# Optimization experiments

Measured on AMD Instinct MI355X. Metric: run time of the kernel, lower is better.

## Reference

```python
import jax, jax.numpy as jnp
import numpy as np

F_NODES = 16384   # number of function nodes
DEG = 8           # in-degree == out-degree per function node
E = F_NODES * DEG # edge-latent dimension (num edges)
B = 64            # batch
H = 16            # hidden_channels of each per-node MLP
LAYERS = 10       # GSNN layers (weights shared across layers)


def setup_inputs() -> dict:
    key = jax.random.key(0)
    k0, k1, k2, k3 = jax.random.split(key, 4)
    x0 = jax.random.normal(k0, (B, E), dtype=jnp.float32)
    # each edge has exactly one destination function node -> in_ixs is a permutation of edges
    in_ixs = jax.random.permutation(k1, E).reshape(F_NODES, DEG)
    # per-node 2-layer MLP weights: in_degree -> H -> out_degree
    W1 = jax.random.normal(k2, (F_NODES, H, DEG), dtype=jnp.float32) * (1.0 / np.sqrt(DEG))
    b1 = jnp.zeros((F_NODES, H), dtype=jnp.float32)
    W2 = jax.random.normal(k3, (F_NODES, DEG, H), dtype=jnp.float32) * (1.0 / np.sqrt(H))
    b2 = jnp.zeros((F_NODES, DEG), dtype=jnp.float32)
    return {"x0": x0, "W1": W1, "b1": b1, "W2": W2, "b2": b2, "in_ixs": in_ixs}


def reference(x0, W1, b1, W2, b2, in_ixs):
    # x0: [B, E] edge-latent input. Each layer: every function node gathers its
    # in-edges, applies its own small MLP, scatters to its out-edges; results are
    # summed into x_new and a residual x0 is added (GSNN.forward).
    x = x0
    for _ in range(LAYERS):
        g = x[:, in_ixs]                                   # [B, F, DEG] gather in-edge values
        h = jax.nn.elu(jnp.einsum('bfd,fhd->bfh', g, W1) + b1)  # [B, F, H]
        o = jnp.einsum('bfh,foh->bfo', h, W2) + b2         # [B, F, DEG]
        # out-edges of node f are the contiguous slots f*DEG:(f+1)*DEG (disjoint scatter)
        x = o.reshape(x0.shape) + x0                       # sum of node scatters + residual
    return x
```

## Files before the change

### kernel.cpp

```cpp
#include <hip/hip_runtime.h>
#include <math.h>

#define F_NODES 16384
#define DEG 8
#define E_TOT (F_NODES * DEG)
#define B 64
#define H 16
#define LAYERS 10
#define NPW 2

typedef unsigned short bf16_t;

__device__ __forceinline__ bf16_t f32_to_bf16(float f)
{
    unsigned u = __float_as_uint(f);
    u = (u + 0x7FFFu + ((u >> 16) & 1u)) >> 16;
    return (bf16_t)u;
}
__device__ __forceinline__ float bf16_to_f32(bf16_t h)
{
    return __uint_as_float((unsigned)h << 16);
}
__device__ __forceinline__ float bfu_lo(unsigned u) { return __uint_as_float(u << 16); }
__device__ __forceinline__ float bfu_hi(unsigned u) { return __uint_as_float(u & 0xFFFF0000u); }

__device__ __forceinline__ float fast_elu(float x)
{
    float e = __builtin_amdgcn_exp2f(x * 1.44269504088896340736f) - 1.0f;
    return x > 0.0f ? x : e;
}

__global__ __launch_bounds__(256) void transpose_in_kernel(
    const float* __restrict__ x0, bf16_t* __restrict__ xT16)
{
    __shared__ float tile[64 * 65];
    const int e0 = blockIdx.x * 64;
    const int c  = threadIdx.x & 63;
    const int r  = threadIdx.x >> 6;

    #pragma unroll
    for (int i = 0; i < 16; ++i) {
        const int b = r + i * 4;
        tile[c * 65 + b] = x0[(size_t)b * E_TOT + e0 + c];
    }
    __syncthreads();
    const int b = threadIdx.x & 63;
    #pragma unroll
    for (int i = 0; i < 16; ++i) {
        const int el = r + i * 4;
        xT16[(size_t)(e0 + el) * B + b] = f32_to_bf16(tile[el * 65 + b]);
    }
}

__global__ __launch_bounds__(256) void build_inv_kernel(
    const int* __restrict__ in_ixs, int* __restrict__ inv)
{
    const int k = blockIdx.x * 256 + threadIdx.x;
    inv[in_ixs[k]] = k;
}

__global__ __launch_bounds__(256) void pack_weights_kernel(
    const float* __restrict__ W1, const float* __restrict__ W2,
    unsigned* __restrict__ W1b, unsigned* __restrict__ W2b)
{
    const int i = blockIdx.x * 256 + threadIdx.x;
    float2 a = ((const float2*)W1)[i];
    W1b[i] = (unsigned)f32_to_bf16(a.x) | ((unsigned)f32_to_bf16(a.y) << 16);
    float2 c = ((const float2*)W2)[i];
    W2b[i] = (unsigned)f32_to_bf16(c.x) | ((unsigned)f32_to_bf16(c.y) << 16);
}

template <int MODE>
__global__ __launch_bounds__(256) void layer_kernel(
    const bf16_t*  __restrict__ zin,
    const bf16_t*  __restrict__ x0T16,
    const unsigned* __restrict__ W1b,
    const float*   __restrict__ b1,
    const unsigned* __restrict__ W2b,
    const float*   __restrict__ b2,
    const int*     __restrict__ in_ixs,
    const int*     __restrict__ inv,
    bf16_t* __restrict__ zout,
    float*  __restrict__ out)
{
    const int lane    = threadIdx.x & 63;
    const int wv      = threadIdx.x >> 6;
    const int wave_id = (int)blockIdx.x * 4 + wv;
    const int f0      = __builtin_amdgcn_readfirstlane(wave_id * NPW);

    float g[NPW][DEG], r[NPW][DEG];
    {
        if (MODE == 0) {
            const int* ixp = in_ixs + f0 * DEG;
            #pragma unroll
            for (int n = 0; n < NPW; ++n)
                #pragma unroll
                for (int d = 0; d < DEG; ++d)
                    g[n][d] = bf16_to_f32(
                        x0T16[(size_t)ixp[n * DEG + d] * B + lane]);
        } else {
            const bf16_t* zp = zin + (size_t)f0 * DEG * B + lane;
            #pragma unroll
            for (int n = 0; n < NPW; ++n)
                #pragma unroll
                for (int d = 0; d < DEG; ++d)
                    g[n][d] = bf16_to_f32(zp[(n * DEG + d) * B]);
        }
        const bf16_t* rp = x0T16 + (size_t)f0 * DEG * B + lane;
        #pragma unroll
        for (int n = 0; n < NPW; ++n)
            #pragma unroll
            for (int d = 0; d < DEG; ++d)
                r[n][d] = bf16_to_f32(rp[(n * DEG + d) * B]);
    }

    #pragma unroll
    for (int n = 0; n < NPW; ++n) {
        const int f = f0 + n;

        const unsigned* w1 = W1b + f * (H * DEG / 2);
        const float*   bb1 = b1 + f * H;
        float h[H];
        #pragma unroll
        for (int j = 0; j < H; ++j) {
            float acc = bb1[j];
            #pragma unroll
            for (int dp = 0; dp < DEG / 2; ++dp) {
                const unsigned u = w1[j * (DEG / 2) + dp];
                acc = fmaf(bfu_lo(u), g[n][2 * dp],     acc);
                acc = fmaf(bfu_hi(u), g[n][2 * dp + 1], acc);
            }
            h[j] = fast_elu(acc);
        }

        const unsigned* w2 = W2b + f * (DEG * H / 2);
        const float*   bb2 = b2 + f * DEG;
        float o[DEG];
        #pragma unroll
        for (int d = 0; d < DEG; ++d) {
            float acc = bb2[d];
            #pragma unroll
            for (int jp = 0; jp < H / 2; ++jp) {
                const unsigned u = w2[d * (H / 2) + jp];
                acc = fmaf(bfu_lo(u), h[2 * jp],     acc);
                acc = fmaf(bfu_hi(u), h[2 * jp + 1], acc);
            }
            o[d] = acc + r[n][d];
        }

        if (MODE == 2) {
            float4 v0 = make_float4(o[0], o[1], o[2], o[3]);
            float4 v1 = make_float4(o[4], o[5], o[6], o[7]);
            float4* dst = (float4*)(out + (size_t)lane * E_TOT + f * DEG);
            dst[0] = v0;
            dst[1] = v1;
        } else {
            const int* invp = inv + f * DEG;
            #pragma unroll
            for (int d = 0; d < DEG; ++d)
                zout[(size_t)invp[d] * B + lane] = f32_to_bf16(o[d]);
        }
    }
}

extern "C" void kernel_launch(void* const* d_in, const int* in_sizes, int n_in,
                              void* d_out, int out_size, void* d_ws, size_t ws_size,
                              hipStream_t stream)
{
    const float* x0     = (const float*)d_in[0];
    const float* W1     = (const float*)d_in[1];
    const float* b1     = (const float*)d_in[2];
    const float* W2     = (const float*)d_in[3];
    const float* b2     = (const float*)d_in[4];
    const int*   in_ixs = (const int*)d_in[5];
    float* out = (float*)d_out;

    const size_t NEL = (size_t)E_TOT * B;
    bf16_t*   x0T16 = (bf16_t*)d_ws;
    bf16_t*   zA    = x0T16 + NEL;
    bf16_t*   zB    = zA + NEL;
    int*      inv   = (int*)(zB + NEL);
    unsigned* W1b   = (unsigned*)(inv + E_TOT);
    unsigned* W2b   = W1b + F_NODES * H * DEG / 2;

    transpose_in_kernel<<<E_TOT / 64, 256, 0, stream>>>(x0, x0T16);
    build_inv_kernel<<<E_TOT / 256, 256, 0, stream>>>(in_ixs, inv);
    pack_weights_kernel<<<F_NODES * H * DEG / 2 / 256, 256, 0, stream>>>(
        W1, W2, W1b, W2b);

    const int grid = F_NODES / (4 * NPW);

    layer_kernel<0><<<grid, 256, 0, stream>>>(
        nullptr, x0T16, W1b, b1, W2b, b2, in_ixs, inv, zA, nullptr);

    const bf16_t* cur = zA;
    bf16_t* nxt = zB;
    for (int l = 1; l < LAYERS - 1; ++l) {
        layer_kernel<1><<<grid, 256, 0, stream>>>(
            cur, x0T16, W1b, b1, W2b, b2, in_ixs, inv, nxt, nullptr);
        cur = nxt;
        nxt = (nxt == zA) ? zB : zA;
    }

    layer_kernel<2><<<grid, 256, 0, stream>>>(
        cur, x0T16, W1b, b1, W2b, b2, in_ixs, inv, nullptr, out);
}
```

Before: 311.3 us.

## Stage contiguous edge loads via LDS with 16-byte vector reads and coalesce final output

The layer kernel now reads the contiguous z and residual slices with 16-byte uint4 loads into per-wave shared memory and unpacks them from LDS, replacing the strided 2-byte global loads. In the final layer the fp32 output is transposed through a padded shared tile so each thread writes contiguous float4 runs along the edge dimension. A minimum-occupancy hint is added to launch_bounds. This aims to cut the number of global memory transactions, at the cost of extra LDS traffic and a block barrier in the last layer.

```diff
diff --git a/kernel.cpp b/kernel.cpp
--- a/kernel.cpp
+++ b/kernel.cpp
@@ -71,7 +71,7 @@
 }
 
 template <int MODE>
-__global__ __launch_bounds__(256) void layer_kernel(
+__global__ __launch_bounds__(256, 4) void layer_kernel(
     const bf16_t*  __restrict__ zin,
     const bf16_t*  __restrict__ x0T16,
     const unsigned* __restrict__ W1b,
@@ -83,41 +83,54 @@
     bf16_t* __restrict__ zout,
     float*  __restrict__ out)
 {
+    __shared__ uint4 stage[4][NPW][2][64];
+
     const int lane    = threadIdx.x & 63;
     const int wv      = threadIdx.x >> 6;
     const int wave_id = (int)blockIdx.x * 4 + wv;
     const int f0      = __builtin_amdgcn_readfirstlane(wave_id * NPW);
 
-    float g[NPW][DEG], r[NPW][DEG];
     {
-        if (MODE == 0) {
-            const int* ixp = in_ixs + f0 * DEG;
-            #pragma unroll
-            for (int n = 0; n < NPW; ++n)
-                #pragma unroll
-                for (int d = 0; d < DEG; ++d)
-                    g[n][d] = bf16_to_f32(
-                        x0T16[(size_t)ixp[n * DEG + d] * B + lane]);
-        } else {
-            const bf16_t* zp = zin + (size_t)f0 * DEG * B + lane;
-            #pragma unroll
-            for (int n = 0; n < NPW; ++n)
-                #pragma unroll
-                for (int d = 0; d < DEG; ++d)
-                    g[n][d] = bf16_to_f32(zp[(n * DEG + d) * B]);
-        }
-        const bf16_t* rp = x0T16 + (size_t)f0 * DEG * B + lane;
+        const uint4* rsrc = (const uint4*)(x0T16 + (size_t)f0 * DEG * B);
+        uint4 r0 = rsrc[lane];
+        uint4 r1 = rsrc[64 + lane];
+        if (MODE != 0) {
+            const uint4* zsrc = (const uint4*)(zin + (size_t)f0 * DEG * B);
+            uint4 z0 = zsrc[lane];
+            uint4 z1 = zsrc[64 + lane];
+            stage[wv][0][0][lane] = z0;
+            stage[wv][1][0][lane] = z1;
+        }
+        stage[wv][0][1][lane] = r0;
+        stage[wv][1][1][lane] = r1;
+    }
+
+    float g0[NPW][DEG];
+    if (MODE == 0) {
+        const int* ixp = in_ixs + f0 * DEG;
         #pragma unroll
         for (int n = 0; n < NPW; ++n)
             #pragma unroll
             for (int d = 0; d < DEG; ++d)
-                r[n][d] = bf16_to_f32(rp[(n * DEG + d) * B]);
-    }
+                g0[n][d] = bf16_to_f32(
+                    x0T16[(size_t)ixp[n * DEG + d] * B + lane]);
+    }
+
+    float oacc[NPW][DEG];
 
     #pragma unroll
     for (int n = 0; n < NPW; ++n) {
         const int f = f0 + n;
 
+        const bf16_t* zb = (const bf16_t*)&stage[wv][n][0][0];
+        const bf16_t* rb = (const bf16_t*)&stage[wv][n][1][0];
+        float g[DEG], r[DEG];
+        #pragma unroll
+        for (int d = 0; d < DEG; ++d) {
+            g[d] = (MODE == 0) ? g0[n][d] : bf16_to_f32(zb[d * 64 + lane]);
+            r[d] = bf16_to_f32(rb[d * 64 + lane]);
+        }
+
         const unsigned* w1 = W1b + f * (H * DEG / 2);
         const float*   bb1 = b1 + f * H;
         float h[H];
@@ -127,15 +140,14 @@
             #pragma unroll
             for (int dp = 0; dp < DEG / 2; ++dp) {
                 const unsigned u = w1[j * (DEG / 2) + dp];
-                acc = fmaf(bfu_lo(u), g[n][2 * dp],     acc);
-                acc = fmaf(bfu_hi(u), g[n][2 * dp + 1], acc);
+                acc = fmaf(bfu_lo(u), g[2 * dp],     acc);
+                acc = fmaf(bfu_hi(u), g[2 * dp + 1], acc);
             }
             h[j] = fast_elu(acc);
         }
 
         const unsigned* w2 = W2b + f * (DEG * H / 2);
         const float*   bb2 = b2 + f * DEG;
-        float o[DEG];
         #pragma unroll
         for (int d = 0; d < DEG; ++d) {
             float acc = bb2[d];
@@ -145,20 +157,39 @@
                 acc = fmaf(bfu_lo(u), h[2 * jp],     acc);
                 acc = fmaf(bfu_hi(u), h[2 * jp + 1], acc);
             }
-            o[d] = acc + r[n][d];
-        }
-
-        if (MODE == 2) {
-            float4 v0 = make_float4(o[0], o[1], o[2], o[3]);
-            float4 v1 = make_float4(o[4], o[5], o[6], o[7]);
-            float4* dst = (float4*)(out + (size_t)lane * E_TOT + f * DEG);
-            dst[0] = v0;
-            dst[1] = v1;
-        } else {
+            oacc[n][d] = acc + r[d];
+        }
+
+        if (MODE != 2) {
             const int* invp = inv + f * DEG;
             #pragma unroll
             for (int d = 0; d < DEG; ++d)
-                zout[(size_t)invp[d] * B + lane] = f32_to_bf16(o[d]);
+                zout[(size_t)invp[d] * B + lane] =
+                    f32_to_bf16(oacc[n][d]);
+        }
+    }
+
+    if (MODE == 2) {
+        __shared__ float outs[64 * 65];
+        #pragma unroll
+        for (int n = 0; n < NPW; ++n)
+            #pragma unroll
+            for (int d = 0; d < DEG; ++d)
+                outs[((wv * NPW + n) * DEG + d) * 65 + lane] = oacc[n][d];
+        __syncthreads();
+
+        const int b  = threadIdx.x >> 2;
+        const int c  = threadIdx.x & 3;
+        const int e0 = (int)blockIdx.x * 64;
+        float* dst = out + (size_t)b * E_TOT + e0 + c * 16;
+        #pragma unroll
+        for (int q = 0; q < 4; ++q) {
+            float4 v;
+            v.x = outs[(c * 16 + q * 4 + 0) * 65 + b];
+            v.y = outs[(c * 16 + q * 4 + 1) * 65 + b];
+            v.z = outs[(c * 16 + q * 4 + 2) * 65 + b];
+            v.w = outs[(c * 16 + q * 4 + 3) * 65 + b];
+            ((float4*)dst)[q] = v;
         }
     }
 }
```

Measured after the change: 314.5 us. No clear change (+1.1%).
